# Kernel tuning notes

Hardware: AMD Instinct MI355X
Metric: run time of the kernel (lower is better)

## Reference

```python
import jax, jax.numpy as jnp
import numpy as np

N_USERS = 100000
N_ITEMS = 50000
N = N_USERS + N_ITEMS          # total graph nodes (users + items)
E = 128                        # emb_size
NNZ = 4_800_000                # edges per sparse adjacency (avg degree 32)
B = 4096                       # lookup batch
NL = 3                         # n_layers


def setup_inputs() -> dict:
    key = jax.random.key(0)
    ks = jax.random.split(key, 12)
    user_emb = jax.random.normal(ks[0], (N_USERS, E), jnp.float32) * 0.05
    item_emb = jax.random.normal(ks[1], (N_ITEMS, E), jnp.float32) * 0.05
    # COO edge lists for low-pass and high-pass normalized adjacencies.
    adj_row = jax.random.randint(ks[2], (NNZ,), 0, N)
    adj_col = jax.random.randint(ks[3], (NNZ,), 0, N)
    adj_val = jax.random.uniform(ks[4], (NNZ,), jnp.float32) / 32.0  # ~normalized weights
    hp_row = jax.random.randint(ks[5], (NNZ,), 0, N)
    hp_col = jax.random.randint(ks[6], (NNZ,), 0, N)
    hp_val = jax.random.uniform(ks[7], (NNZ,), jnp.float32) / 32.0
    # per-layer Linear(2E -> E): weight stored as [in, out] so y = x @ W + b
    W = jax.random.normal(ks[8], (NL, 2 * E, E), jnp.float32) * (1.0 / np.sqrt(2 * E))
    b = jnp.zeros((NL, E), jnp.float32)
    users = jax.random.randint(ks[9], (B,), 0, N_USERS)
    items = jax.random.randint(ks[10], (B,), 0, N_ITEMS)
    return dict(user_emb=user_emb, item_emb=item_emb, adj_val=adj_val, hp_val=hp_val,
                W=W, b=b, adj_row=adj_row, adj_col=adj_col,
                hp_row=hp_row, hp_col=hp_col, users=users, items=items)


def spmm(row, col, val, x):
    # sparse [N,N] @ dense [N,E] via gather + segment-sum
    return jax.ops.segment_sum(val[:, None] * x[col], row, num_segments=N)


def reference(user_emb, item_emb, adj_val, hp_val, W, b,
              adj_row, adj_col, hp_row, hp_col, users, items):
    ego = jnp.concatenate([user_emb, item_emb], axis=0)  # [N, E]
    pos = ego
    dis = ego
    for k in range(NL):
        pos = spmm(adj_row, adj_col, adj_val, pos)       # low-pass propagation
        dis = spmm(hp_row, hp_col, hp_val, dis)          # high-pass propagation
        ego = jnp.concatenate([pos, dis], axis=1) @ W[k] + b[k]  # [N, E]
        pos = ego
        dis = ego
    user_out = ego[users]                 # ego[:N_USERS][users]
    item_out = ego[N_USERS + items]       # ego[N_USERS:][items]
    return (user_out, item_out)
```

## Files before the change

### kernel.cpp

```cpp
#include <hip/hip_runtime.h>

#define N_USERS 100000
#define N_ITEMS 50000
#define NTOT    150000
#define E       128
#define NNZ     4800000
#define BATCH   4096
#define TILE    16
#define BSH     10
#define BROWS   1024
#define NBK     147
#define SLOT    16

typedef int v4i __attribute__((ext_vector_type(4)));

__device__ __forceinline__ int   ldnt_i(const int* p)   { return __builtin_nontemporal_load(p); }
__device__ __forceinline__ float ldnt_f(const float* p) { return __builtin_nontemporal_load(p); }
__device__ __forceinline__ v4i   ld_v4(const void* p)   { return *(const v4i*)p; }

__global__ __launch_bounds__(1024) void bucket_count(const int* __restrict__ rowA,
                                                     const int* __restrict__ rowH,
                                                     int* __restrict__ cntA,
                                                     int* __restrict__ cntH) {
    __shared__ int c[2 * NBK];
    for (int i = threadIdx.x; i < 2 * NBK; i += 1024) c[i] = 0;
    __syncthreads();
    int i = blockIdx.x * 1024 + threadIdx.x;
    const int stride = gridDim.x * 1024;
    for (; i < NNZ; i += stride) {
        atomicAdd(&c[ldnt_i(rowA + i) >> BSH], 1);
        atomicAdd(&c[NBK + (ldnt_i(rowH + i) >> BSH)], 1);
    }
    __syncthreads();
    for (int j = threadIdx.x; j < 2 * NBK; j += 1024) {
        const int v = c[j];
        if (v) atomicAdd(j < NBK ? (cntA + j) : (cntH + (j - NBK)), v);
    }
}

__global__ __launch_bounds__(64) void bucket_scan(const int* __restrict__ cntA,
                                                  const int* __restrict__ cntH,
                                                  int* __restrict__ baseA, int* __restrict__ baseH,
                                                  int* __restrict__ gcurA, int* __restrict__ gcurH) {
    const int t = threadIdx.x;
    if (t == 0) {
        int run = 0;
        for (int j = 0; j < NBK; ++j) { baseA[j] = run; gcurA[j] = run; run += cntA[j]; }
        baseA[NBK] = run;
    } else if (t == 1) {
        int run = 0;
        for (int j = 0; j < NBK; ++j) { baseH[j] = run; gcurH[j] = run; run += cntH[j]; }
        baseH[NBK] = run;
    }
}

__global__ __launch_bounds__(1024) void wc_scatter(const int* __restrict__ rowA, const int* __restrict__ colA,
                                                   const float* __restrict__ valA,
                                                   const int* __restrict__ rowH, const int* __restrict__ colH,
                                                   const float* __restrict__ valH,
                                                   int* __restrict__ gcurA, int* __restrict__ gcurH,
                                                   int2* __restrict__ stA, int2* __restrict__ stH) {
    __shared__ int  lcnt[2 * NBK];
    __shared__ int2 lent[2 * NBK * SLOT];
    for (int i = threadIdx.x; i < 2 * NBK; i += 1024) lcnt[i] = 0;
    __syncthreads();
    const int stride = gridDim.x * 1024;
    const int rounds = (NNZ + stride - 1) / stride;
    for (int rd = 0; rd < rounds; ++rd) {
        const int i = rd * stride + blockIdx.x * 1024 + threadIdx.x;
        if (i < NNZ) {
            {
                const int r = ldnt_i(rowA + i), cc = ldnt_i(colA + i);
                const float v = ldnt_f(valA + i);
                const int b = r >> BSH;
                const int2 pk = make_int2(((r & (BROWS - 1)) << 18) | cc, __float_as_int(v));
                const int n = atomicAdd(&lcnt[b], 1);
                if (n < SLOT) lent[b * SLOT + n] = pk;
                else          stA[atomicAdd(&gcurA[b], 1)] = pk;
            }
            {
                const int r = ldnt_i(rowH + i), cc = ldnt_i(colH + i);
                const float v = ldnt_f(valH + i);
                const int b = r >> BSH;
                const int gb = NBK + b;
                const int2 pk = make_int2(((r & (BROWS - 1)) << 18) | cc, __float_as_int(v));
                const int n = atomicAdd(&lcnt[gb], 1);
                if (n < SLOT) lent[gb * SLOT + n] = pk;
                else          stH[atomicAdd(&gcurH[b], 1)] = pk;
            }
        }
        __syncthreads();
        const int thresh = (rd == rounds - 1) ? 1 : 8;
        for (int gb = threadIdx.x; gb < 2 * NBK; gb += 1024) {
            int n = lcnt[gb]; if (n > SLOT) n = SLOT;
            if (n >= thresh) {
                int*  gc = (gb < NBK) ? &gcurA[gb] : &gcurH[gb - NBK];
                int2* st = (gb < NBK) ? stA : stH;
                const int p = atomicAdd(gc, n);
                for (int j = 0; j < n; ++j) st[p + j] = lent[gb * SLOT + j];
                lcnt[gb] = 0;
            }
        }
        __syncthreads();
    }
}

__global__ __launch_bounds__(1024) void bucket_csr(const int2* __restrict__ stA, const int2* __restrict__ stH,
                                                   const int* __restrict__ baseA, const int* __restrict__ baseH,
                                                   int* __restrict__ rpA, int* __restrict__ rpH,
                                                   int2* __restrict__ edA, int2* __restrict__ edH) {
    const int isH = blockIdx.x >= NBK;
    const int b   = isH ? blockIdx.x - NBK : blockIdx.x;
    const int2* st   = isH ? stH   : stA;
    const int*  base = isH ? baseH : baseA;
    int*  rp = isH ? rpH : rpA;
    int2* ed = isH ? edH : edA;
    const int s = base[b], e = base[b + 1];
    const int t = threadIdx.x, lane = t & 63, wv = t >> 6;
    __shared__ int cnt[BROWS];
    __shared__ int wsum[16], woff[16];
    cnt[t] = 0;
    __syncthreads();
    for (int i = s + t; i < e; i += 1024) atomicAdd(&cnt[st[i].x >> 18], 1);
    __syncthreads();
    const int v = cnt[t];
    int x = v;
    #pragma unroll
    for (int off = 1; off < 64; off <<= 1) {
        const int n = __shfl_up(x, off);
        if (lane >= off) x += n;
    }
    if (lane == 63) wsum[wv] = x;
    __syncthreads();
    if (t == 0) { int acc = 0; for (int w = 0; w < 16; ++w) { woff[w] = acc; acc += wsum[w]; } }
    __syncthreads();
    const int excl = woff[wv] + (x - v);
    const int rglob = (b << BSH) + t;
    if (rglob < NTOT) rp[rglob] = s + excl;
    __syncthreads();
    cnt[t] = excl;
    __syncthreads();
    for (int i = s + t; i < e; i += 1024) {
        const int2 pk = st[i];
        const int rl = pk.x >> 18;
        const int p = s + atomicAdd(&cnt[rl], 1);
        ed[p] = make_int2(pk.x & 0x3FFFF, pk.y);
    }
    if (t == 0 && b == 0) rp[NTOT] = NNZ;
}

__global__ __launch_bounds__(256) void copy_int(const int* __restrict__ src,
                                                int* __restrict__ dst, int n) {
    const int i = blockIdx.x * blockDim.x + threadIdx.x;
    if (i < n) dst[i] = src[i];
}

template<bool FIRST>
__device__ __forceinline__ const float* rowb(int c, const float* __restrict__ ue,
                                             const float* __restrict__ ie,
                                             const float* __restrict__ A) {
    if constexpr (FIRST)
        return (c < N_USERS) ? (ue + (size_t)c * E) : (ie + (size_t)(c - N_USERS) * E);
    else
        return A + (size_t)c * E;
}

template<bool FIRST, int HALF>
__device__ __forceinline__ void pf_half(v4i q, const float* __restrict__ ue,
                                        const float* __restrict__ ie,
                                        const float* __restrict__ A,
                                        int sub, int half, float2& acc) {
    const int   c = half ? q[2] : q[0];
    const float v = __int_as_float(half ? q[3] : q[1]);
    const float2 xv = ((const float2*)(rowb<FIRST>(c, ue, ie, A) + HALF * 64))[sub];
    acc.x = fmaf(v, xv.x, acc.x);
    acc.y = fmaf(v, xv.y, acc.y);
}

template<bool FIRST, int HALF>
__device__ __forceinline__ float2 accum_half(int s, int e, const int2* __restrict__ ed,
                                             const float* __restrict__ ue,
                                             const float* __restrict__ ie,
                                             const float* __restrict__ A,
                                             int sub, int half) {
    float2 a{0.f, 0.f}, b{0.f, 0.f};
    int i = s;
    if (i < e && (i & 1)) {
        const int2 t0 = ed[i];
        const float v = half ? 0.f : __int_as_float(t0.y);
        const float2 xv = ((const float2*)(rowb<FIRST>(t0.x, ue, ie, A) + HALF * 64))[sub];
        a.x = fmaf(v, xv.x, a.x); a.y = fmaf(v, xv.y, a.y);
        ++i;
    }
    for (; i + 7 < e; i += 8) {
        const v4i q0 = ld_v4(ed + i);
        const v4i q1 = ld_v4(ed + i + 2);
        const v4i q2 = ld_v4(ed + i + 4);
        const v4i q3 = ld_v4(ed + i + 6);
        pf_half<FIRST, HALF>(q0, ue, ie, A, sub, half, a);
        pf_half<FIRST, HALF>(q1, ue, ie, A, sub, half, b);
        pf_half<FIRST, HALF>(q2, ue, ie, A, sub, half, a);
        pf_half<FIRST, HALF>(q3, ue, ie, A, sub, half, b);
    }
    for (; i + 1 < e; i += 2) {
        const v4i q = ld_v4(ed + i);
        pf_half<FIRST, HALF>(q, ue, ie, A, sub, half, a);
    }
    if (i < e) {
        const int2 t0 = ed[i];
        const float v = half ? 0.f : __int_as_float(t0.y);
        const float2 xv = ((const float2*)(rowb<FIRST>(t0.x, ue, ie, A) + HALF * 64))[sub];
        a.x = fmaf(v, xv.x, a.x); a.y = fmaf(v, xv.y, a.y);
    }
    return make_float2(a.x + b.x, a.y + b.y);
}

template<bool FIRST>
__global__ __launch_bounds__(256) void fused_passA(
    const float* __restrict__ A,
    const float* __restrict__ ue, const float* __restrict__ ie,
    const int* __restrict__ rpA, const int2* __restrict__ edA,
    const int* __restrict__ rpH, const int2* __restrict__ edH,
    float* __restrict__ outb) {
    const int t = threadIdx.x, lane = t & 63, sub = lane & 31, half = lane >> 5, wv = t >> 6;
    const int r0 = blockIdx.x * TILE;
    #pragma unroll
    for (int rl = 0; rl < 4; ++rl) {
        const int r = r0 + wv * 4 + rl;
        const float2 ap = accum_half<FIRST, 0>(rpA[r], rpA[r + 1], edA, ue, ie, A, sub, half);
        const float2 ad = accum_half<FIRST, 0>(rpH[r], rpH[r + 1], edH, ue, ie, A, sub, half);
        float2 send = half ? ap : ad;
        float2 recv;
        recv.x = __shfl_xor(send.x, 32);
        recv.y = __shfl_xor(send.y, 32);
        if (!half) {
            const float2 f{ap.x + recv.x, ap.y + recv.y};
            ((float2*)(outb + (size_t)r * E))[sub] = f;
        } else {
            const float2 f{ad.x + recv.x, ad.y + recv.y};
            ((float2*)(outb + (size_t)r * E + 64))[sub] = f;
        }
    }
}

template<bool FIRST>
__global__ __launch_bounds__(256) void fused_passB(
    const float* __restrict__ A,
    const float* __restrict__ ue, const float* __restrict__ ie,
    const int* __restrict__ rpA, const int2* __restrict__ edA,
    const int* __restrict__ rpH, const int2* __restrict__ edH,
    const float* __restrict__ Wk, const float* __restrict__ bk,
    float* __restrict__ outb) {
    __shared__ float sP[TILE][E];
    __shared__ float sD[TILE][E];
    const int t = threadIdx.x, lane = t & 63, sub = lane & 31, half = lane >> 5, wv = t >> 6;
    const int r0 = blockIdx.x * TILE;
    #pragma unroll
    for (int rl = 0; rl < 4; ++rl) {
        const int r = r0 + wv * 4 + rl;
        const float2 ap = accum_half<FIRST, 1>(rpA[r], rpA[r + 1], edA, ue, ie, A, sub, half);
        const float2 ad = accum_half<FIRST, 1>(rpH[r], rpH[r + 1], edH, ue, ie, A, sub, half);
        float2 send = half ? ap : ad;
        float2 recv;
        recv.x = __shfl_xor(send.x, 32);
        recv.y = __shfl_xor(send.y, 32);
        if (!half) {
            const float2 f{ap.x + recv.x, ap.y + recv.y};
            ((float2*)&sP[wv * 4 + rl][64])[sub] = f;
        } else {
            const float2 f{ad.x + recv.x, ad.y + recv.y};
            ((float2*)&sD[wv * 4 + rl][64])[sub] = f;
        }
    }
    {
        const int row = t >> 4;
        const int q   = t & 15;
        const float4 vp = *(const float4*)(outb + (size_t)(r0 + row) * E + q * 4);
        const float4 vd = *(const float4*)(outb + (size_t)(r0 + row) * E + 64 + q * 4);
        *(float4*)&sP[row][q * 4] = vp;
        *(float4*)&sD[row][q * 4] = vd;
    }
    __syncthreads();

    const int j = t & (E - 1);
    const int h = t >> 7;
    float acc[8];
    const float bj = bk[j];
    #pragma unroll
    for (int rr = 0; rr < 8; ++rr) acc[rr] = bj;
    #pragma unroll 4
    for (int i = 0; i < E; ++i) {
        const float w = Wk[(size_t)i * E + j];
        #pragma unroll
        for (int rr = 0; rr < 8; ++rr) acc[rr] = fmaf(sP[h * 8 + rr][i], w, acc[rr]);
    }
    #pragma unroll 4
    for (int i = 0; i < E; ++i) {
        const float w = Wk[(size_t)(E + i) * E + j];
        #pragma unroll
        for (int rr = 0; rr < 8; ++rr) acc[rr] = fmaf(sD[h * 8 + rr][i], w, acc[rr]);
    }
    #pragma unroll
    for (int rr = 0; rr < 8; ++rr)
        outb[(size_t)(r0 + h * 8 + rr) * E + j] = acc[rr];
}

__device__ __forceinline__ void pf_full(v4i q, const float* __restrict__ A,
                                        int sub, int half, float4& acc) {
    const int   c = half ? q[2] : q[0];
    const float v = __int_as_float(half ? q[3] : q[1]);
    const float4 xv = ((const float4*)(A + (size_t)c * E))[sub];
    acc.x = fmaf(v, xv.x, acc.x);
    acc.y = fmaf(v, xv.y, acc.y);
    acc.z = fmaf(v, xv.z, acc.z);
    acc.w = fmaf(v, xv.w, acc.w);
}

__device__ __forceinline__ float4 accum_full(int s, int e, const int2* __restrict__ ed,
                                             const float* __restrict__ A, int sub, int half) {
    float4 a{0.f,0.f,0.f,0.f}, b{0.f,0.f,0.f,0.f};
    int i = s;
    if (i < e && (i & 1)) {
        const int2 t0 = ed[i];
        const float v = half ? 0.f : __int_as_float(t0.y);
        const float4 xv = ((const float4*)(A + (size_t)t0.x * E))[sub];
        a.x = fmaf(v, xv.x, a.x); a.y = fmaf(v, xv.y, a.y);
        a.z = fmaf(v, xv.z, a.z); a.w = fmaf(v, xv.w, a.w);
        ++i;
    }
    for (; i + 7 < e; i += 8) {
        const v4i q0 = ld_v4(ed + i);
        const v4i q1 = ld_v4(ed + i + 2);
        const v4i q2 = ld_v4(ed + i + 4);
        const v4i q3 = ld_v4(ed + i + 6);
        pf_full(q0, A, sub, half, a);
        pf_full(q1, A, sub, half, b);
        pf_full(q2, A, sub, half, a);
        pf_full(q3, A, sub, half, b);
    }
    for (; i + 1 < e; i += 2) {
        const v4i q = ld_v4(ed + i);
        pf_full(q, A, sub, half, a);
    }
    if (i < e) {
        const int2 t0 = ed[i];
        const float v = half ? 0.f : __int_as_float(t0.y);
        const float4 xv = ((const float4*)(A + (size_t)t0.x * E))[sub];
        a.x = fmaf(v, xv.x, a.x); a.y = fmaf(v, xv.y, a.y);
        a.z = fmaf(v, xv.z, a.z); a.w = fmaf(v, xv.w, a.w);
    }
    return make_float4(a.x + b.x, a.y + b.y, a.z + b.z, a.w + b.w);
}

__global__ __launch_bounds__(256) void fused_final(
    const float* __restrict__ A,
    const int* __restrict__ rpA, const int2* __restrict__ edA,
    const int* __restrict__ rpH, const int2* __restrict__ edH,
    const float* __restrict__ Wk, const float* __restrict__ bk,
    const int* __restrict__ users, const int* __restrict__ items,
    float* __restrict__ out) {
    __shared__ float sP[TILE][E];
    __shared__ float sD[TILE][E];
    const int t = threadIdx.x, lane = t & 63, sub = lane & 31, half = lane >> 5, wv = t >> 6;

    #pragma unroll
    for (int rl = 0; rl < 4; ++rl) {
        const int slot = blockIdx.x * TILE + wv * 4 + rl;
        const int r = (slot < BATCH) ? users[slot] : (N_USERS + items[slot - BATCH]);
        const float4 ap = accum_full(rpA[r], rpA[r + 1], edA, A, sub, half);
        const float4 ad = accum_full(rpH[r], rpH[r + 1], edH, A, sub, half);
        float4 send = half ? ap : ad;
        float4 recv;
        recv.x = __shfl_xor(send.x, 32);
        recv.y = __shfl_xor(send.y, 32);
        recv.z = __shfl_xor(send.z, 32);
        recv.w = __shfl_xor(send.w, 32);
        if (!half) {
            ((float4*)&sP[wv * 4 + rl][0])[sub] = make_float4(ap.x + recv.x, ap.y + recv.y,
                                                              ap.z + recv.z, ap.w + recv.w);
        } else {
            ((float4*)&sD[wv * 4 + rl][0])[sub] = make_float4(ad.x + recv.x, ad.y + recv.y,
                                                              ad.z + recv.z, ad.w + recv.w);
        }
    }
    __syncthreads();

    const int j = t & (E - 1);
    const int h = t >> 7;
    float acc[8];
    const float bj = bk[j];
    #pragma unroll
    for (int rr = 0; rr < 8; ++rr) acc[rr] = bj;
    #pragma unroll 4
    for (int i = 0; i < E; ++i) {
        const float w = Wk[(size_t)i * E + j];
        #pragma unroll
        for (int rr = 0; rr < 8; ++rr) acc[rr] = fmaf(sP[h * 8 + rr][i], w, acc[rr]);
    }
    #pragma unroll 4
    for (int i = 0; i < E; ++i) {
        const float w = Wk[(size_t)(E + i) * E + j];
        #pragma unroll
        for (int rr = 0; rr < 8; ++rr) acc[rr] = fmaf(sD[h * 8 + rr][i], w, acc[rr]);
    }
    #pragma unroll
    for (int rr = 0; rr < 8; ++rr)
        out[(size_t)(blockIdx.x * TILE + h * 8 + rr) * E + j] = acc[rr];
}

extern "C" void kernel_launch(void* const* d_in, const int* in_sizes, int n_in,
                              void* d_out, int out_size, void* d_ws, size_t ws_size,
                              hipStream_t stream) {
    const float* user_emb = (const float*)d_in[0];
    const float* item_emb = (const float*)d_in[1];
    const float* adj_val  = (const float*)d_in[2];
    const float* hp_val   = (const float*)d_in[3];
    const float* W        = (const float*)d_in[4];
    const float* bias     = (const float*)d_in[5];
    const int*   adj_row  = (const int*)d_in[6];
    const int*   adj_col  = (const int*)d_in[7];
    const int*   hp_row   = (const int*)d_in[8];
    const int*   hp_col   = (const int*)d_in[9];
    const int*   users    = (const int*)d_in[10];
    const int*   items    = (const int*)d_in[11];
    float* out = (float*)d_out;

    float* buf0 = (float*)d_ws;
    float* buf1 = buf0 + (size_t)NTOT * E;
    int2*  edA  = (int2*)(buf1 + (size_t)NTOT * E);
    int2*  edH  = edA + NNZ;
    int2*  stA  = (int2*)buf0;
    int2*  stH  = stA + NNZ;

    int* rpA   = (int*)d_out;
    int* rpH   = rpA + (NTOT + 1);
    int* cntA  = rpH + (NTOT + 1);
    int* cntH  = cntA + NBK;
    int* baseA = cntH + NBK;
    int* baseH = baseA + (NBK + 1);
    int* gcurA = baseH + (NBK + 1);
    int* gcurH = gcurA + NBK;

    int* rpA2 = (int*)buf1;
    int* rpH2 = rpA2 + (NTOT + 1);

    hipMemsetAsync(cntA, 0, (size_t)2 * NBK * sizeof(int), stream);
    bucket_count<<<512, 1024, 0, stream>>>(adj_row, hp_row, cntA, cntH);
    bucket_scan<<<1, 64, 0, stream>>>(cntA, cntH, baseA, baseH, gcurA, gcurH);
    wc_scatter<<<512, 1024, 0, stream>>>(adj_row, adj_col, adj_val,
                                         hp_row, hp_col, hp_val,
                                         gcurA, gcurH, stA, stH);
    bucket_csr<<<2 * NBK, 1024, 0, stream>>>(stA, stH, baseA, baseH, rpA, rpH, edA, edH);

    const int gridF = NTOT / TILE;
    const int gridL = (2 * BATCH) / TILE;

    fused_passA<true><<<gridF, 256, 0, stream>>>(
        nullptr, user_emb, item_emb, rpA, edA, rpH, edH, buf1);
    fused_passB<true><<<gridF, 256, 0, stream>>>(
        nullptr, user_emb, item_emb, rpA, edA, rpH, edH, W, bias, buf1);
    fused_passA<false><<<gridF, 256, 0, stream>>>(
        buf1, nullptr, nullptr, rpA, edA, rpH, edH, buf0);
    fused_passB<false><<<gridF, 256, 0, stream>>>(
        buf1, nullptr, nullptr, rpA, edA, rpH, edH,
        W + (size_t)2 * E * E, bias + E, buf0);

    copy_int<<<(2 * (NTOT + 1) + 255) / 256, 256, 0, stream>>>(rpA, rpA2, 2 * (NTOT + 1));
    fused_final<<<gridL, 256, 0, stream>>>(
        buf0, rpA2, edA, rpH2, edH,
        W + (size_t)4 * E * E, bias + 2 * E, users, items, out);
}
```

Baseline: 2.050 ms.

## Merge split half-column SpMM passes into one full-row fused layer kernel

The first two layers previously ran two kernels each: one gathering the low 64 columns of neighbour rows and writing them to a global buffer, and one gathering the high 64 columns, reloading the first half and applying the linear layer. Both are replaced by a single kernel in which each lane gathers a float4 covering the full 128-wide row, keeps results in shared memory, and then does the matmul. This removes a kernel launch, one extra read of the CSR structure and the intermediate global round-trip, and uses wider gathers. The trade-off is a larger per-pass gather footprint that the split had likely been chosen to keep cache-resident.

Result: faster. 1.818 ms (-11.3%).

```diff
diff --git a/kernel.cpp b/kernel.cpp
--- a/kernel.cpp
+++ b/kernel.cpp
@@ -156,40 +156,48 @@
 }
 
 template<bool FIRST>
-__device__ __forceinline__ const float* rowb(int c, const float* __restrict__ ue,
-                                             const float* __restrict__ ie,
-                                             const float* __restrict__ A) {
+__device__ __forceinline__ const float4* rowbase(int c, const float* __restrict__ ue,
+                                                 const float* __restrict__ ie,
+                                                 const float* __restrict__ A) {
     if constexpr (FIRST)
-        return (c < N_USERS) ? (ue + (size_t)c * E) : (ie + (size_t)(c - N_USERS) * E);
+        return (c < N_USERS) ? ((const float4*)ue + (size_t)c * (E / 4))
+                             : ((const float4*)ie + (size_t)(c - N_USERS) * (E / 4));
     else
-        return A + (size_t)c * E;
-}
-
-template<bool FIRST, int HALF>
-__device__ __forceinline__ void pf_half(v4i q, const float* __restrict__ ue,
+        return (const float4*)A + (size_t)c * (E / 4);
+}
+
+template<bool FIRST>
+__device__ __forceinline__ void pairfma(v4i q, const float* __restrict__ ue,
                                         const float* __restrict__ ie,
                                         const float* __restrict__ A,
-                                        int sub, int half, float2& acc) {
+                                        int sub, int half, float4& acc) {
     const int   c = half ? q[2] : q[0];
     const float v = __int_as_float(half ? q[3] : q[1]);
-    const float2 xv = ((const float2*)(rowb<FIRST>(c, ue, ie, A) + HALF * 64))[sub];
+    const float4 xv = rowbase<FIRST>(c, ue, ie, A)[sub];
     acc.x = fmaf(v, xv.x, acc.x);
     acc.y = fmaf(v, xv.y, acc.y);
-}
-
-template<bool FIRST, int HALF>
-__device__ __forceinline__ float2 accum_half(int s, int e, const int2* __restrict__ ed,
-                                             const float* __restrict__ ue,
-                                             const float* __restrict__ ie,
-                                             const float* __restrict__ A,
-                                             int sub, int half) {
-    float2 a{0.f, 0.f}, b{0.f, 0.f};
+    acc.z = fmaf(v, xv.z, acc.z);
+    acc.w = fmaf(v, xv.w, acc.w);
+}
+
+template<bool FIRST>
+__device__ __forceinline__ float4 row_accum(const int* __restrict__ rp,
+                                            const int2* __restrict__ ed,
+                                            const float* __restrict__ ue,
+                                            const float* __restrict__ ie,
+                                            const float* __restrict__ A,
+                                            int r, int sub, int half) {
+    const int s = rp[r];
+    const int e = rp[r + 1];
+    float4 accA = {0.f, 0.f, 0.f, 0.f};
+    float4 accB = {0.f, 0.f, 0.f, 0.f};
     int i = s;
     if (i < e && (i & 1)) {
         const int2 t0 = ed[i];
         const float v = half ? 0.f : __int_as_float(t0.y);
-        const float2 xv = ((const float2*)(rowb<FIRST>(t0.x, ue, ie, A) + HALF * 64))[sub];
-        a.x = fmaf(v, xv.x, a.x); a.y = fmaf(v, xv.y, a.y);
+        const float4 xv = rowbase<FIRST>(t0.x, ue, ie, A)[sub];
+        accA.x = fmaf(v, xv.x, accA.x); accA.y = fmaf(v, xv.y, accA.y);
+        accA.z = fmaf(v, xv.z, accA.z); accA.w = fmaf(v, xv.w, accA.w);
         ++i;
     }
     for (; i + 7 < e; i += 8) {
@@ -197,88 +205,61 @@
         const v4i q1 = ld_v4(ed + i + 2);
         const v4i q2 = ld_v4(ed + i + 4);
         const v4i q3 = ld_v4(ed + i + 6);
-        pf_half<FIRST, HALF>(q0, ue, ie, A, sub, half, a);
-        pf_half<FIRST, HALF>(q1, ue, ie, A, sub, half, b);
-        pf_half<FIRST, HALF>(q2, ue, ie, A, sub, half, a);
-        pf_half<FIRST, HALF>(q3, ue, ie, A, sub, half, b);
+        pairfma<FIRST>(q0, ue, ie, A, sub, half, accA);
+        pairfma<FIRST>(q1, ue, ie, A, sub, half, accB);
+        pairfma<FIRST>(q2, ue, ie, A, sub, half, accA);
+        pairfma<FIRST>(q3, ue, ie, A, sub, half, accB);
     }
     for (; i + 1 < e; i += 2) {
         const v4i q = ld_v4(ed + i);
-        pf_half<FIRST, HALF>(q, ue, ie, A, sub, half, a);
+        pairfma<FIRST>(q, ue, ie, A, sub, half, accA);
     }
     if (i < e) {
         const int2 t0 = ed[i];
         const float v = half ? 0.f : __int_as_float(t0.y);
-        const float2 xv = ((const float2*)(rowb<FIRST>(t0.x, ue, ie, A) + HALF * 64))[sub];
-        a.x = fmaf(v, xv.x, a.x); a.y = fmaf(v, xv.y, a.y);
-    }
-    return make_float2(a.x + b.x, a.y + b.y);
+        const float4 xv = rowbase<FIRST>(t0.x, ue, ie, A)[sub];
+        accA.x = fmaf(v, xv.x, accA.x); accA.y = fmaf(v, xv.y, accA.y);
+        accA.z = fmaf(v, xv.z, accA.z); accA.w = fmaf(v, xv.w, accA.w);
+    }
+    return make_float4(accA.x + accB.x, accA.y + accB.y,
+                       accA.z + accB.z, accA.w + accB.w);
 }
 
 template<bool FIRST>
-__global__ __launch_bounds__(256) void fused_passA(
-    const float* __restrict__ A,
-    const float* __restrict__ ue, const float* __restrict__ ie,
-    const int* __restrict__ rpA, const int2* __restrict__ edA,
-    const int* __restrict__ rpH, const int2* __restrict__ edH,
-    float* __restrict__ outb) {
-    const int t = threadIdx.x, lane = t & 63, sub = lane & 31, half = lane >> 5, wv = t >> 6;
-    const int r0 = blockIdx.x * TILE;
-    #pragma unroll
-    for (int rl = 0; rl < 4; ++rl) {
-        const int r = r0 + wv * 4 + rl;
-        const float2 ap = accum_half<FIRST, 0>(rpA[r], rpA[r + 1], edA, ue, ie, A, sub, half);
-        const float2 ad = accum_half<FIRST, 0>(rpH[r], rpH[r + 1], edH, ue, ie, A, sub, half);
-        float2 send = half ? ap : ad;
-        float2 recv;
-        recv.x = __shfl_xor(send.x, 32);
-        recv.y = __shfl_xor(send.y, 32);
-        if (!half) {
-            const float2 f{ap.x + recv.x, ap.y + recv.y};
-            ((float2*)(outb + (size_t)r * E))[sub] = f;
-        } else {
-            const float2 f{ad.x + recv.x, ad.y + recv.y};
-            ((float2*)(outb + (size_t)r * E + 64))[sub] = f;
-        }
-    }
-}
-
-template<bool FIRST>
-__global__ __launch_bounds__(256) void fused_passB(
+__global__ __launch_bounds__(256) void fused_layer(
     const float* __restrict__ A,
     const float* __restrict__ ue, const float* __restrict__ ie,
     const int* __restrict__ rpA, const int2* __restrict__ edA,
     const int* __restrict__ rpH, const int2* __restrict__ edH,
     const float* __restrict__ Wk, const float* __restrict__ bk,
-    float* __restrict__ outb) {
+    float* __restrict__ out) {
     __shared__ float sP[TILE][E];
     __shared__ float sD[TILE][E];
-    const int t = threadIdx.x, lane = t & 63, sub = lane & 31, half = lane >> 5, wv = t >> 6;
-    const int r0 = blockIdx.x * TILE;
+    const int t    = threadIdx.x;
+    const int lane = t & 63;
+    const int sub  = lane & 31;
+    const int half = lane >> 5;
+    const int wv   = t >> 6;
+    const int r0   = blockIdx.x * TILE;
+
     #pragma unroll
     for (int rl = 0; rl < 4; ++rl) {
         const int r = r0 + wv * 4 + rl;
-        const float2 ap = accum_half<FIRST, 1>(rpA[r], rpA[r + 1], edA, ue, ie, A, sub, half);
-        const float2 ad = accum_half<FIRST, 1>(rpH[r], rpH[r + 1], edH, ue, ie, A, sub, half);
-        float2 send = half ? ap : ad;
-        float2 recv;
+        const float4 ap = row_accum<FIRST>(rpA, edA, ue, ie, A, r, sub, half);
+        const float4 ad = row_accum<FIRST>(rpH, edH, ue, ie, A, r, sub, half);
+        float4 send = half ? ap : ad;
+        float4 recv;
         recv.x = __shfl_xor(send.x, 32);
         recv.y = __shfl_xor(send.y, 32);
+        recv.z = __shfl_xor(send.z, 32);
+        recv.w = __shfl_xor(send.w, 32);
         if (!half) {
-            const float2 f{ap.x + recv.x, ap.y + recv.y};
-            ((float2*)&sP[wv * 4 + rl][64])[sub] = f;
+            ((float4*)&sP[wv * 4 + rl][0])[sub] = make_float4(ap.x + recv.x, ap.y + recv.y,
+                                                              ap.z + recv.z, ap.w + recv.w);
         } else {
-            const float2 f{ad.x + recv.x, ad.y + recv.y};
-            ((float2*)&sD[wv * 4 + rl][64])[sub] = f;
+            ((float4*)&sD[wv * 4 + rl][0])[sub] = make_float4(ad.x + recv.x, ad.y + recv.y,
+                                                              ad.z + recv.z, ad.w + recv.w);
         }
-    }
-    {
-        const int row = t >> 4;
-        const int q   = t & 15;
-        const float4 vp = *(const float4*)(outb + (size_t)(r0 + row) * E + q * 4);
-        const float4 vd = *(const float4*)(outb + (size_t)(r0 + row) * E + 64 + q * 4);
-        *(float4*)&sP[row][q * 4] = vp;
-        *(float4*)&sD[row][q * 4] = vd;
     }
     __syncthreads();
 
@@ -302,7 +283,7 @@
     }
     #pragma unroll
     for (int rr = 0; rr < 8; ++rr)
-        outb[(size_t)(r0 + h * 8 + rr) * E + j] = acc[rr];
+        out[(size_t)(r0 + h * 8 + rr) * E + j] = acc[rr];
 }
 
 __device__ __forceinline__ void pf_full(v4i q, const float* __restrict__ A,
@@ -455,13 +436,9 @@
     const int gridF = NTOT / TILE;
     const int gridL = (2 * BATCH) / TILE;
 
-    fused_passA<true><<<gridF, 256, 0, stream>>>(
-        nullptr, user_emb, item_emb, rpA, edA, rpH, edH, buf1);
-    fused_passB<true><<<gridF, 256, 0, stream>>>(
+    fused_layer<true><<<gridF, 256, 0, stream>>>(
         nullptr, user_emb, item_emb, rpA, edA, rpH, edH, W, bias, buf1);
-    fused_passA<false><<<gridF, 256, 0, stream>>>(
-        buf1, nullptr, nullptr, rpA, edA, rpH, edH, buf0);
-    fused_passB<false><<<gridF, 256, 0, stream>>>(
+    fused_layer<false><<<gridF, 256, 0, stream>>>(
         buf1, nullptr, nullptr, rpA, edA, rpH, edH,
         W + (size_t)2 * E * E, bias + E, buf0);
 
```
